# Kernel optimization log

Hardware: AMD Instinct MI355X
Metric: run time of the kernel (lower is better)

## Reference

```python
import jax, jax.numpy as jnp
from jax import lax
import numpy as np

# dims
B, C, H, W, T = 8, 2, 64, 64, 200
# per-layer neuron configs (defaults from NetworkBasic.__init__)
THETA = (30.0, 50.0, 100.0)
TAU_SR = (1.0, 2.0, 4.0)
TAU_REF = (1.0, 2.0, 4.0)
SCALE_REF = (1.0, 1.0, 1.0)
TAU_RHO = (1.0, 1.0, 10.0)


def psp(x, tau):
    """SLAYER synaptic response: first-order leaky integration over time axis (last).
    a[t] = exp(-1/tau) * a[t-1] + x[t]"""
    d = jnp.exp(jnp.asarray(-1.0 / tau, x.dtype))
    xt = jnp.moveaxis(x, -1, 0)  # [T, B, C, H, W]
    def step(a, xi):
        a = d * a + xi
        return a, a
    _, ys = lax.scan(step, jnp.zeros_like(xt[0]), xt)
    return jnp.moveaxis(ys, 0, -1)


def spike(u, theta, tau_ref, scale_ref, tau_rho):
    """SLAYER spiking unit: threshold + leaky refractory state, sequential over T.
    Forward emits hard spikes; surrogate (sigmoid) used only for gradients."""
    dref = jnp.exp(jnp.asarray(-1.0 / tau_ref, u.dtype))
    th = jnp.asarray(theta, u.dtype)
    ut = jnp.moveaxis(u, -1, 0)  # [T, ...]
    def step(r, ui):
        v = ui + r
        hard = (v >= th).astype(u.dtype)
        sur = jax.nn.sigmoid((v - th) / tau_rho)
        s = sur + lax.stop_gradient(hard - sur)  # straight-through surrogate
        r2 = dref * r - th * scale_ref * s       # refractory subtraction
        return r2, s
    _, s = lax.scan(step, jnp.zeros_like(ut[0]), ut)
    return jnp.moveaxis(s, 0, -1)


def conv2d_t(x, w, pad):
    """slayer.conv: spatial conv applied independently per timestep (kernel kxkx1, no bias)."""
    Bb, Cc, Hh, Ww, Tt = x.shape
    xt = jnp.moveaxis(x, -1, 1).reshape(Bb * Tt, Cc, Hh, Ww)
    y = lax.conv_general_dilated(xt, w, (1, 1), [(pad, pad), (pad, pad)],
                                 dimension_numbers=("NCHW", "OIHW", "NCHW"))
    O = w.shape[0]
    return jnp.moveaxis(y.reshape(Bb, Tt, O, Hh, Ww), 1, -1)


def convT2d_t(x, w):
    """slayer.convTranspose kernel=2 stride=2, per timestep (exact 2x upsample)."""
    Bb, Cc, Hh, Ww, Tt = x.shape
    xt = jnp.moveaxis(x, -1, 1).reshape(Bb * Tt, Cc, Hh, Ww)
    y = lax.conv_transpose(xt, w, (2, 2), "VALID",
                           dimension_numbers=("NCHW", "OIHW", "NCHW"))
    O = w.shape[0]
    return jnp.moveaxis(y.reshape(Bb, Tt, O, 2 * Hh, 2 * Ww), 1, -1)


def setup_inputs() -> dict:
    key = jax.random.key(0)
    k0, k1, k2, k3 = jax.random.split(key, 4)
    spikeInput = (jax.random.uniform(k0, (B, C, H, W, T)) < 0.3).astype(jnp.float32)
    w1 = jax.random.normal(k1, (8, 2, 5, 5), jnp.float32) * 10.0
    w2 = jax.random.normal(k2, (8, 8, 3, 3), jnp.float32) * 10.0
    wup = jax.random.normal(k3, (2, 8, 2, 2), jnp.float32) * 10.0
    return {"spikeInput": spikeInput, "w1": w1, "w2": w2, "wup": wup}


def reference(spikeInput, w1, w2, wup):
    Bb, Cc, Hh, Ww, Tt = spikeInput.shape
    psp1 = psp(spikeInput, TAU_SR[0])
    psp1_up = jax.image.resize(psp1, (Bb, Cc, 2 * Hh, 2 * Ww, Tt), method="linear")
    s1 = spike(conv2d_t(psp1, w1, 2), THETA[0], TAU_REF[0], SCALE_REF[0], TAU_RHO[0])
    s2 = spike(conv2d_t(psp(s1, TAU_SR[1]), w2, 1), THETA[1], TAU_REF[1], SCALE_REF[1], TAU_RHO[1])
    s3 = spike(convT2d_t(psp(s2, TAU_SR[2]), wup) + psp1_up,
               THETA[2], TAU_REF[2], SCALE_REF[2], TAU_RHO[2])
    return s3
```

## Files before the change

kernel.cpp:

```cpp
#include <hip/hip_runtime.h>

#define DEC1 0.36787944117144233f
#define DEC2 0.60653065971263342f
#define DEC3 0.77880078307140487f

typedef float v2f __attribute__((ext_vector_type(2)));

__global__ void prep_weights(const float* __restrict__ w1,
                             const float* __restrict__ w2,
                             const float* __restrict__ wup,
                             float* __restrict__ wr)
{
    int i = blockIdx.x * 256 + threadIdx.x;
    if (i < 400) {
        int o = i & 7, tap = i >> 3;
        int c = tap / 25, rem = tap % 25, ky = rem / 5, kx = rem % 5;
        wr[i] = w1[((o * 2 + c) * 5 + ky) * 5 + kx];
    }
    if (i < 576) {
        int o = i & 7, tap = i >> 3;
        int c = tap / 9, rem = tap % 9, ky = rem / 3, kx = rem % 3;
        wr[400 + i] = w2[((o * 8 + c) * 3 + ky) * 3 + kx];
    }
    if (i < 64) {
        int c = i & 7, r = i >> 3;
        int dj = r & 1, di = (r >> 1) & 1, o = r >> 2;
        wr[976 + i] = wup[((o * 8 + c) * 2 + (1 - di)) * 2 + (1 - dj)];
    }
}

static __device__ __forceinline__ float4 spike_psp4(float4 u, float th, float dref,
                                                    float dq, float& r, float& q)
{
    float4 qv; float v, s;
    v = __fadd_rn(u.x, r); s = (v >= th) ? 1.f : 0.f;
    r = __fsub_rn(__fmul_rn(dref, r), __fmul_rn(th, s));
    q = __fadd_rn(__fmul_rn(dq, q), s); qv.x = q;
    v = __fadd_rn(u.y, r); s = (v >= th) ? 1.f : 0.f;
    r = __fsub_rn(__fmul_rn(dref, r), __fmul_rn(th, s));
    q = __fadd_rn(__fmul_rn(dq, q), s); qv.y = q;
    v = __fadd_rn(u.z, r); s = (v >= th) ? 1.f : 0.f;
    r = __fsub_rn(__fmul_rn(dref, r), __fmul_rn(th, s));
    q = __fadd_rn(__fmul_rn(dq, q), s); qv.z = q;
    v = __fadd_rn(u.w, r); s = (v >= th) ? 1.f : 0.f;
    r = __fsub_rn(__fmul_rn(dref, r), __fmul_rn(th, s));
    q = __fadd_rn(__fmul_rn(dq, q), s); qv.w = q;
    return qv;
}

static __device__ __forceinline__ float4 spike4(float4 u, float th, float dref, float& r)
{
    float4 ov; float v, s;
    v = __fadd_rn(u.x, r); s = (v >= th) ? 1.f : 0.f;
    r = __fsub_rn(__fmul_rn(dref, r), __fmul_rn(th, s)); ov.x = s;
    v = __fadd_rn(u.y, r); s = (v >= th) ? 1.f : 0.f;
    r = __fsub_rn(__fmul_rn(dref, r), __fmul_rn(th, s)); ov.y = s;
    v = __fadd_rn(u.z, r); s = (v >= th) ? 1.f : 0.f;
    r = __fsub_rn(__fmul_rn(dref, r), __fmul_rn(th, s)); ov.z = s;
    v = __fadd_rn(u.w, r); s = (v >= th) ? 1.f : 0.f;
    r = __fsub_rn(__fmul_rn(dref, r), __fmul_rn(th, s)); ov.w = s;
    return ov;
}

#define PKFMA(ALO_, AHI_, WV_, DLO_, DHI_) { \
    v2f wv2_ = { (WV_), (WV_) }; \
    ALO_ = __builtin_elementwise_fma(wv2_, DLO_, ALO_); \
    AHI_ = __builtin_elementwise_fma(wv2_, DHI_, AHI_); }

#define PSP4(V_, X_, st) { \
    V_.x = __fadd_rn(__fmul_rn(DEC1, st),   X_.x); \
    V_.y = __fadd_rn(__fmul_rn(DEC1, V_.x), X_.y); \
    V_.z = __fadd_rn(__fmul_rn(DEC1, V_.y), X_.z); \
    V_.w = __fadd_rn(__fmul_rn(DEC1, V_.z), X_.w); st = V_.w; }

__global__ __launch_bounds__(256, 2)
void snn_fused(const float* __restrict__ spk,
               const float* __restrict__ wr,
               float* __restrict__ out)
{
    const int tid  = threadIdx.x;
    const int b    = blockIdx.x >> 6;
    const int tile = blockIdx.x & 63;
    const int gy0  = (tile >> 3) << 3;
    const int gx0  = (tile & 7) << 3;

    __shared__ float4 sP1[2][2][2][224];
    __shared__ float4 sP2[8][2][100];
    __shared__ float4 sP3[8][2][64];

    float aP0 = 0.f, aP1 = 0.f;
    float rB[4], qB[4];
    float rC[2] = {0.f, 0.f}, qC[2] = {0.f, 0.f};
    float r3[2] = {0.f, 0.f};
#pragma unroll
    for (int i = 0; i < 4; ++i) { rB[i] = 0.f; qB[i] = 0.f; }

    const int ary = tid / 14, arx = tid % 14;
    const int aidx = ary * 16 + arx;
    const int aiy = gy0 - 3 + ary, aix = gx0 - 3 + arx;
    const bool avalid = (tid < 196) && (aiy >= 0) && (aiy < 64) && (aix >= 0) && (aix < 64);
    const int aoff0 = avalid ? (((b * 2 + 0) * 64 + aiy) * 64 + aix) * 200 : 0;
    const int aoff1 = avalid ? (((b * 2 + 1) * 64 + aiy) * 64 + aix) * 200 : 0;

    const int bh   = __builtin_amdgcn_readfirstlane(tid >> 7);
    const int bpx  = tid & 127;
    int by_, bx_;
    if (bpx < 80) { by_ = bpx >> 3; bx_ = bpx & 7; }
    else          { int t2 = bpx - 80; by_ = t2 >> 1; bx_ = 8 + (t2 & 1); }
    const int by = by_, bx = bx_;
    const int bwr = by * 10 + bx;
    const int ochB = tid >> 7;

    const int ch2  = __builtin_amdgcn_readfirstlane(tid >> 7);
    const int cop  = __builtin_amdgcn_readfirstlane(tid >> 6) & 1;
    const int cpx  = tid & 63;
    const int cy   = cpx >> 3, cx = cpx & 7;
    const int och2 = (tid >> 6) * 2;

    const int od  = tid >> 7;
    const int ddi = (tid >> 6) & 1;
    const int dpx = tid & 63;
    const int dy  = dpx >> 3, dxx = dpx & 7;
    const int diy = gy0 + dy, dix = gx0 + dxx;

    const float ay  = ddi ? ((diy == 63) ? 1.f : 0.75f) : ((diy == 0) ? 0.f : 0.25f);
    const float byw = ddi ? ((diy == 63) ? 0.f : 0.25f) : ((diy == 0) ? 1.f : 0.75f);
    const float ax0 = (dix == 0)  ? 0.f : 0.25f;
    const float bx0 = (dix == 0)  ? 1.f : 0.75f;
    const float ax1 = (dix == 63) ? 1.f : 0.75f;
    const float bx1 = (dix == 63) ? 0.f : 0.25f;
    const int   didx = (dy + 2 + ddi) * 16 + (dxx + 2);

    float4 x00 = make_float4(0.f,0.f,0.f,0.f), x01 = x00, x10 = x00, x11 = x00;
    if (avalid) {
        x00 = *(const float4*)(spk + aoff0);
        x01 = *(const float4*)(spk + aoff0 + 4);
        x10 = *(const float4*)(spk + aoff1);
        x11 = *(const float4*)(spk + aoff1 + 4);
    }

#pragma unroll 1
    for (int ck = 0; ck < 25; ++ck) {
        const int t0 = ck * 8;
        const int p  = ck & 1;

        if (tid < 196) {
            float4 v;
            PSP4(v, x00, aP0); sP1[p][0][0][aidx] = v;
            PSP4(v, x01, aP0); sP1[p][0][1][aidx] = v;
            PSP4(v, x10, aP1); sP1[p][1][0][aidx] = v;
            PSP4(v, x11, aP1); sP1[p][1][1][aidx] = v;
            if (ck < 24 && avalid) {
                x00 = *(const float4*)(spk + aoff0 + t0 + 8);
                x01 = *(const float4*)(spk + aoff0 + t0 + 12);
                x10 = *(const float4*)(spk + aoff1 + t0 + 8);
                x11 = *(const float4*)(spk + aoff1 + t0 + 12);
            }
        }
        __syncthreads();

        if (bpx < 100) {
            v2f alo[8], ahi[8];
#pragma unroll
            for (int o = 0; o < 8; ++o) { alo[o] = (v2f)(0.f); ahi[o] = (v2f)(0.f); }
#pragma unroll 1
            for (int c = 0; c < 2; ++c) {
#pragma unroll 1
                for (int ky = 0; ky < 5; ++ky) {
                    const float4* r0 = &sP1[p][c][bh][(by + ky) * 16 + bx];
                    const float*  wrow = wr + (c * 25 + ky * 5) * 8;
#pragma unroll
                    for (int kx = 0; kx < 5; ++kx) {
                        float4 d = r0[kx];
                        v2f dlo = { d.x, d.y }, dhi = { d.z, d.w };
#pragma unroll
                        for (int o = 0; o < 8; ++o) {
                            float wv = wrow[kx * 8 + o];
                            PKFMA(alo[o], ahi[o], wv, dlo, dhi);
                        }
                    }
                }
            }
#pragma unroll
            for (int o = 0; o < 8; ++o)
                sP2[o][bh][bwr] = make_float4(alo[o].x, alo[o].y, ahi[o].x, ahi[o].y);
        }
        __syncthreads();

        if (bpx < 100) {
#pragma unroll
            for (int j = 0; j < 4; ++j) {
                const int o = ochB * 4 + j;
                float4 u0 = sP2[o][0][bwr];
                float4 u1 = sP2[o][1][bwr];
                float4 q0 = spike_psp4(u0, 30.f, DEC1, DEC2, rB[j], qB[j]);
                sP2[o][0][bwr] = q0;
                float4 q1 = spike_psp4(u1, 30.f, DEC1, DEC2, rB[j], qB[j]);
                sP2[o][1][bwr] = q1;
            }
        }
        __syncthreads();

        {
            v2f alo[4], ahi[4];
#pragma unroll
            for (int j = 0; j < 4; ++j) { alo[j] = (v2f)(0.f); ahi[j] = (v2f)(0.f); }
            const float* wC = wr + 400 + cop * 4;
#pragma unroll 1
            for (int c = 0; c < 8; ++c) {
#pragma unroll 1
                for (int ky = 0; ky < 3; ++ky) {
                    const float4* r0 = &sP2[c][ch2][(cy + ky) * 10 + cx];
                    const float*  wrow = wC + (c * 9 + ky * 3) * 8;
#pragma unroll
                    for (int kx = 0; kx < 3; ++kx) {
                        float4 d = r0[kx];
                        v2f dlo = { d.x, d.y }, dhi = { d.z, d.w };
#pragma unroll
                        for (int j = 0; j < 4; ++j) {
                            float wv = wrow[kx * 8 + j];
                            PKFMA(alo[j], ahi[j], wv, dlo, dhi);
                        }
                    }
                }
            }
#pragma unroll
            for (int j = 0; j < 4; ++j)
                sP3[cop * 4 + j][ch2][cpx] =
                    make_float4(alo[j].x, alo[j].y, ahi[j].x, ahi[j].y);
        }
        __syncthreads();

        {
#pragma unroll
            for (int j = 0; j < 2; ++j) {
                const int o = och2 + j;
                float4 u0 = sP3[o][0][cpx];
                float4 u1 = sP3[o][1][cpx];
                float4 q0 = spike_psp4(u0, 50.f, DEC2, DEC3, rC[j], qC[j]);
                sP3[o][0][cpx] = q0;
                float4 q1 = spike_psp4(u1, 50.f, DEC2, DEC3, rC[j], qC[j]);
                sP3[o][1][cpx] = q1;
            }
        }
        __syncthreads();

        {
#pragma unroll 1
            for (int h = 0; h < 2; ++h) {
                float4 p3[8];
#pragma unroll
                for (int c = 0; c < 8; ++c) p3[c] = sP3[c][h][dpx];
                float4 P0a = sP1[p][od][h][didx];
                float4 P0b = sP1[p][od][h][didx + 1];
                float4 P0c = sP1[p][od][h][didx + 2];
                float4 P1a = sP1[p][od][h][didx + 16];
                float4 P1b = sP1[p][od][h][didx + 17];
                float4 P1c = sP1[p][od][h][didx + 18];
#pragma unroll
                for (int dj = 0; dj < 2; ++dj) {
                    const float ax  = dj ? ax1 : ax0;
                    const float bxw = dj ? bx1 : bx0;
                    v2f tlo = (v2f)(0.f), thi = (v2f)(0.f);
                    const float* wD = wr + 976 + ((od * 2 + ddi) * 2 + dj) * 8;
#pragma unroll
                    for (int c = 0; c < 8; ++c) {
                        float wv = wD[c];
                        v2f dlo = { p3[c].x, p3[c].y }, dhi = { p3[c].z, p3[c].w };
                        PKFMA(tlo, thi, wv, dlo, dhi);
                    }
                    float4 tv = make_float4(tlo.x, tlo.y, thi.x, thi.y);
                    float4 A  = dj ? P0b : P0a;
                    float4 Bv = dj ? P0c : P0b;
                    float4 Cv = dj ? P1b : P1a;
                    float4 Dv = dj ? P1c : P1b;
                    float4 up, u; float ra, rb;
                    ra = __fadd_rn(__fmul_rn(ay, A.x),  __fmul_rn(byw, Cv.x));
                    rb = __fadd_rn(__fmul_rn(ay, Bv.x), __fmul_rn(byw, Dv.x));
                    up.x = __fadd_rn(__fmul_rn(ax, ra), __fmul_rn(bxw, rb));
                    ra = __fadd_rn(__fmul_rn(ay, A.y),  __fmul_rn(byw, Cv.y));
                    rb = __fadd_rn(__fmul_rn(ay, Bv.y), __fmul_rn(byw, Dv.y));
                    up.y = __fadd_rn(__fmul_rn(ax, ra), __fmul_rn(bxw, rb));
                    ra = __fadd_rn(__fmul_rn(ay, A.z),  __fmul_rn(byw, Cv.z));
                    rb = __fadd_rn(__fmul_rn(ay, Bv.z), __fmul_rn(byw, Dv.z));
                    up.z = __fadd_rn(__fmul_rn(ax, ra), __fmul_rn(bxw, rb));
                    ra = __fadd_rn(__fmul_rn(ay, A.w),  __fmul_rn(byw, Cv.w));
                    rb = __fadd_rn(__fmul_rn(ay, Bv.w), __fmul_rn(byw, Dv.w));
                    up.w = __fadd_rn(__fmul_rn(ax, ra), __fmul_rn(bxw, rb));
                    u.x = __fadd_rn(tv.x, up.x);
                    u.y = __fadd_rn(tv.y, up.y);
                    u.z = __fadd_rn(tv.z, up.z);
                    u.w = __fadd_rn(tv.w, up.w);
                    float4 ov = spike4(u, 100.f, DEC3, r3[dj]);
                    float* op = out + ((((b * 2 + od) * 128 + (2 * diy + ddi)) * 128)
                                       + (2 * dix + dj)) * 200 + t0 + h * 4;
                    *(float4*)op = ov;
                }
            }
        }
    }
}

extern "C" void kernel_launch(void* const* d_in, const int* in_sizes, int n_in,
                              void* d_out, int out_size, void* d_ws, size_t ws_size,
                              hipStream_t stream)
{
    const float* spk = (const float*)d_in[0];
    const float* w1  = (const float*)d_in[1];
    const float* w2  = (const float*)d_in[2];
    const float* wup = (const float*)d_in[3];
    float* outp = (float*)d_out;
    float* wr   = (float*)d_ws;

    prep_weights<<<dim3(3), dim3(256), 0, stream>>>(w1, w2, wup, wr);
    snn_fused<<<dim3(512), dim3(256), 0, stream>>>(spk, wr, outp);
}
```

Measured before the change: 569.1 us.

## Stage weights in LDS and software-pipeline conv tap loads with sched barriers

Copies the reordered weights into shared memory once per block and reads them as float4 vectors instead of scalar global loads. The two conv inner loops are restructured into double-buffered register pipelines: the next row's data and weights are prefetched while the current row's packed FMAs execute, with scheduling barriers to keep the overlap in place. The transposed-conv weights are hoisted out of the inner loop and output offsets are precomputed. This raises register pressure, which at the launch bound of two blocks per SM could cause spills.

```diff
diff --git a/kernel.cpp b/kernel.cpp
--- a/kernel.cpp
+++ b/kernel.cpp
@@ -62,10 +62,10 @@
     return ov;
 }
 
-#define PKFMA(ALO_, AHI_, WV_, DLO_, DHI_) { \
+#define PKQ(AL_, AH_, WV_, DLO_, DHI_) { \
     v2f wv2_ = { (WV_), (WV_) }; \
-    ALO_ = __builtin_elementwise_fma(wv2_, DLO_, ALO_); \
-    AHI_ = __builtin_elementwise_fma(wv2_, DHI_, AHI_); }
+    AL_ = __builtin_elementwise_fma(wv2_, DLO_, AL_); \
+    AH_ = __builtin_elementwise_fma(wv2_, DHI_, AH_); }
 
 #define PSP4(V_, X_, st) { \
     V_.x = __fadd_rn(__fmul_rn(DEC1, st),   X_.x); \
@@ -73,6 +73,35 @@
     V_.z = __fadd_rn(__fmul_rn(DEC1, V_.y), X_.z); \
     V_.w = __fadd_rn(__fmul_rn(DEC1, V_.z), X_.w); st = V_.w; }
 
+#define BTAP(D_, WA_, WB_) { v2f dlo_ = { D_.x, D_.y }, dhi_ = { D_.z, D_.w }; \
+    PKQ(alo[0], ahi[0], WA_.x, dlo_, dhi_); PKQ(alo[1], ahi[1], WA_.y, dlo_, dhi_); \
+    PKQ(alo[2], ahi[2], WA_.z, dlo_, dhi_); PKQ(alo[3], ahi[3], WA_.w, dlo_, dhi_); \
+    PKQ(alo[4], ahi[4], WB_.x, dlo_, dhi_); PKQ(alo[5], ahi[5], WB_.y, dlo_, dhi_); \
+    PKQ(alo[6], ahi[6], WB_.z, dlo_, dhi_); PKQ(alo[7], ahi[7], WB_.w, dlo_, dhi_); }
+#define BROWF(S) { BTAP(S##d0, S##w0, S##w1) BTAP(S##d1, S##w2, S##w3) \
+    BTAP(S##d2, S##w4, S##w5) BTAP(S##d3, S##w6, S##w7) BTAP(S##d4, S##w8, S##w9) }
+#define BPRE(S) { \
+    const float4* rn_ = &sP1[p][nc][bh][(by + nk) * 16 + bx]; \
+    const float4* wq_ = sW4 + wrow; \
+    S##w0 = wq_[0]; S##w1 = wq_[1]; S##w2 = wq_[2]; S##w3 = wq_[3]; \
+    S##w4 = wq_[4]; S##w5 = wq_[5]; S##w6 = wq_[6]; S##w7 = wq_[7]; \
+    S##w8 = wq_[8]; S##w9 = wq_[9]; \
+    S##d0 = rn_[0]; S##d1 = rn_[1]; S##d2 = rn_[2]; S##d3 = rn_[3]; S##d4 = rn_[4]; \
+    ++nk; if (nk == 5) { nk = 0; ++nc; } if (nc == 2) { nc = 1; nk = 4; } \
+    wrow += 10; if (wrow == 100) wrow = 90; }
+
+#define CTAP(D_, WA_) { v2f dlo_ = { D_.x, D_.y }, dhi_ = { D_.z, D_.w }; \
+    PKQ(clo[0], chi[0], WA_.x, dlo_, dhi_); PKQ(clo[1], chi[1], WA_.y, dlo_, dhi_); \
+    PKQ(clo[2], chi[2], WA_.z, dlo_, dhi_); PKQ(clo[3], chi[3], WA_.w, dlo_, dhi_); }
+#define CROWF(S) { CTAP(S##d0, S##w0) CTAP(S##d1, S##w1) CTAP(S##d2, S##w2) }
+#define CPRE(S) { \
+    const float4* rn_ = &sP2[nc2][ch2][(cy + nk2) * 10 + cx]; \
+    const float4* wq_ = sW4 + wrow2; \
+    S##w0 = wq_[cop]; S##w1 = wq_[2 + cop]; S##w2 = wq_[4 + cop]; \
+    S##d0 = rn_[0]; S##d1 = rn_[1]; S##d2 = rn_[2]; \
+    ++nk2; if (nk2 == 3) { nk2 = 0; ++nc2; } if (nc2 == 8) { nc2 = 7; nk2 = 2; } \
+    wrow2 += 6; if (wrow2 == 244) wrow2 = 238; }
+
 __global__ __launch_bounds__(256, 2)
 void snn_fused(const float* __restrict__ spk,
                const float* __restrict__ wr,
@@ -87,6 +116,9 @@
     __shared__ float4 sP1[2][2][2][224];
     __shared__ float4 sP2[8][2][100];
     __shared__ float4 sP3[8][2][64];
+    __shared__ float4 sW4[264];
+
+    for (int i = tid; i < 260; i += 256) sW4[i] = ((const float4*)wr)[i];
 
     float aP0 = 0.f, aP1 = 0.f;
     float rB[4], qB[4];
@@ -130,6 +162,10 @@
     const float ax1 = (dix == 63) ? 1.f : 0.75f;
     const float bx1 = (dix == 63) ? 0.f : 0.25f;
     const int   didx = (dy + 2 + ddi) * 16 + (dxx + 2);
+
+    const int opix0 = (((b * 2 + od) * 128 + (2 * diy + ddi)) * 128 + 2 * dix) * 200;
+    const int opix1 = opix0 + 200;
+    const int kD    = (od * 2 + ddi) * 2;
 
     float4 x00 = make_float4(0.f,0.f,0.f,0.f), x01 = x00, x10 = x00, x11 = x00;
     if (avalid) {
@@ -163,23 +199,20 @@
             v2f alo[8], ahi[8];
 #pragma unroll
             for (int o = 0; o < 8; ++o) { alo[o] = (v2f)(0.f); ahi[o] = (v2f)(0.f); }
+            float4 Ad0, Ad1, Ad2, Ad3, Ad4;
+            float4 Aw0, Aw1, Aw2, Aw3, Aw4, Aw5, Aw6, Aw7, Aw8, Aw9;
+            float4 Bd0, Bd1, Bd2, Bd3, Bd4;
+            float4 Bw0, Bw1, Bw2, Bw3, Bw4, Bw5, Bw6, Bw7, Bw8, Bw9;
+            int nc = 0, nk = 0, wrow = 0;
+            BPRE(A)
 #pragma unroll 1
-            for (int c = 0; c < 2; ++c) {
-#pragma unroll 1
-                for (int ky = 0; ky < 5; ++ky) {
-                    const float4* r0 = &sP1[p][c][bh][(by + ky) * 16 + bx];
-                    const float*  wrow = wr + (c * 25 + ky * 5) * 8;
-#pragma unroll
-                    for (int kx = 0; kx < 5; ++kx) {
-                        float4 d = r0[kx];
-                        v2f dlo = { d.x, d.y }, dhi = { d.z, d.w };
-#pragma unroll
-                        for (int o = 0; o < 8; ++o) {
-                            float wv = wrow[kx * 8 + o];
-                            PKFMA(alo[o], ahi[o], wv, dlo, dhi);
-                        }
-                    }
-                }
+            for (int i = 0; i < 5; ++i) {
+                BPRE(B)
+                __builtin_amdgcn_sched_barrier(0);
+                BROWF(A)
+                BPRE(A)
+                __builtin_amdgcn_sched_barrier(0);
+                BROWF(B)
             }
 #pragma unroll
             for (int o = 0; o < 8; ++o)
@@ -202,32 +235,26 @@
         __syncthreads();
 
         {
-            v2f alo[4], ahi[4];
-#pragma unroll
-            for (int j = 0; j < 4; ++j) { alo[j] = (v2f)(0.f); ahi[j] = (v2f)(0.f); }
-            const float* wC = wr + 400 + cop * 4;
+            v2f clo[4], chi[4];
+#pragma unroll
+            for (int j = 0; j < 4; ++j) { clo[j] = (v2f)(0.f); chi[j] = (v2f)(0.f); }
+            float4 Ed0, Ed1, Ed2, Ew0, Ew1, Ew2;
+            float4 Fd0, Fd1, Fd2, Fw0, Fw1, Fw2;
+            int nc2 = 0, nk2 = 0, wrow2 = 100;
+            CPRE(E)
 #pragma unroll 1
-            for (int c = 0; c < 8; ++c) {
-#pragma unroll 1
-                for (int ky = 0; ky < 3; ++ky) {
-                    const float4* r0 = &sP2[c][ch2][(cy + ky) * 10 + cx];
-                    const float*  wrow = wC + (c * 9 + ky * 3) * 8;
-#pragma unroll
-                    for (int kx = 0; kx < 3; ++kx) {
-                        float4 d = r0[kx];
-                        v2f dlo = { d.x, d.y }, dhi = { d.z, d.w };
-#pragma unroll
-                        for (int j = 0; j < 4; ++j) {
-                            float wv = wrow[kx * 8 + j];
-                            PKFMA(alo[j], ahi[j], wv, dlo, dhi);
-                        }
-                    }
-                }
+            for (int i = 0; i < 12; ++i) {
+                CPRE(F)
+                __builtin_amdgcn_sched_barrier(0);
+                CROWF(E)
+                CPRE(E)
+                __builtin_amdgcn_sched_barrier(0);
+                CROWF(F)
             }
 #pragma unroll
             for (int j = 0; j < 4; ++j)
                 sP3[cop * 4 + j][ch2][cpx] =
-                    make_float4(alo[j].x, alo[j].y, ahi[j].x, ahi[j].y);
+                    make_float4(clo[j].x, clo[j].y, chi[j].x, chi[j].y);
         }
         __syncthreads();
 
@@ -246,6 +273,8 @@
         __syncthreads();
 
         {
+            const float4 wd0a = sW4[244 + kD * 2 + 0], wd0b = sW4[244 + kD * 2 + 1];
+            const float4 wd1a = sW4[244 + kD * 2 + 2], wd1b = sW4[244 + kD * 2 + 3];
 #pragma unroll 1
             for (int h = 0; h < 2; ++h) {
                 float4 p3[8];
@@ -261,14 +290,25 @@
                 for (int dj = 0; dj < 2; ++dj) {
                     const float ax  = dj ? ax1 : ax0;
                     const float bxw = dj ? bx1 : bx0;
+                    const float4 wA = dj ? wd1a : wd0a;
+                    const float4 wB = dj ? wd1b : wd0b;
                     v2f tlo = (v2f)(0.f), thi = (v2f)(0.f);
-                    const float* wD = wr + 976 + ((od * 2 + ddi) * 2 + dj) * 8;
-#pragma unroll
-                    for (int c = 0; c < 8; ++c) {
-                        float wv = wD[c];
-                        v2f dlo = { p3[c].x, p3[c].y }, dhi = { p3[c].z, p3[c].w };
-                        PKFMA(tlo, thi, wv, dlo, dhi);
-                    }
+                    { v2f dlo = { p3[0].x, p3[0].y }, dhi = { p3[0].z, p3[0].w };
+                      PKQ(tlo, thi, wA.x, dlo, dhi); }
+                    { v2f dlo = { p3[1].x, p3[1].y }, dhi = { p3[1].z, p3[1].w };
+                      PKQ(tlo, thi, wA.y, dlo, dhi); }
+                    { v2f dlo = { p3[2].x, p3[2].y }, dhi = { p3[2].z, p3[2].w };
+                      PKQ(tlo, thi, wA.z, dlo, dhi); }
+                    { v2f dlo = { p3[3].x, p3[3].y }, dhi = { p3[3].z, p3[3].w };
+                      PKQ(tlo, thi, wA.w, dlo, dhi); }
+                    { v2f dlo = { p3[4].x, p3[4].y }, dhi = { p3[4].z, p3[4].w };
+                      PKQ(tlo, thi, wB.x, dlo, dhi); }
+                    { v2f dlo = { p3[5].x, p3[5].y }, dhi = { p3[5].z, p3[5].w };
+                      PKQ(tlo, thi, wB.y, dlo, dhi); }
+                    { v2f dlo = { p3[6].x, p3[6].y }, dhi = { p3[6].z, p3[6].w };
+                      PKQ(tlo, thi, wB.z, dlo, dhi); }
+                    { v2f dlo = { p3[7].x, p3[7].y }, dhi = { p3[7].z, p3[7].w };
+                      PKQ(tlo, thi, wB.w, dlo, dhi); }
                     float4 tv = make_float4(tlo.x, tlo.y, thi.x, thi.y);
                     float4 A  = dj ? P0b : P0a;
                     float4 Bv = dj ? P0c : P0b;
@@ -292,8 +332,7 @@
                     u.z = __fadd_rn(tv.z, up.z);
                     u.w = __fadd_rn(tv.w, up.w);
                     float4 ov = spike4(u, 100.f, DEC3, r3[dj]);
-                    float* op = out + ((((b * 2 + od) * 128 + (2 * diy + ddi)) * 128)
-                                       + (2 * dix + dj)) * 200 + t0 + h * 4;
+                    float* op = out + (dj ? opix1 : opix0) + t0 + h * 4;
                     *(float4*)op = ov;
                 }
             }
```

Result: no change. 577.0 us (+1.4%).
